# Kernel optimization log

Hardware: AMD Instinct MI355X
Metric: run time of the kernel (lower is better)

The kernel has to match this reference:

```python
import jax, jax.numpy as jnp
import numpy as np

B, L, D = 4, 896, 2048
HQ, HKV, HD = 32, 8, 64
GROUP = HQ // HKV          # 4
TOKENS_PER_FRAME = 7
ROPE_BASE = 10000.0


def setup_inputs() -> dict:
    key = jax.random.key(0)
    ks = jax.random.split(key, 5)
    s = 0.02
    return {
        "x": jax.random.normal(ks[0], (B, L, D), jnp.float32),
        "wq": jax.random.normal(ks[1], (D, D), jnp.float32) * s,
        "wk": jax.random.normal(ks[2], (D, HKV * HD), jnp.float32) * s,
        "wv": jax.random.normal(ks[3], (D, HKV * HD), jnp.float32) * s,
        "wo": jax.random.normal(ks[4], (D, D), jnp.float32) * s,
        "pos_ids": jnp.arange(L, dtype=jnp.int32),
    }


def _apply_rotary(t, cos, sin):
    # t: [B, L, H, HD]; rotate all HD dims, interleaved pairs.
    Bt, Lt, Ht, Hd = t.shape
    tp = t.reshape(Bt, Lt, Ht, Hd // 2, 2)
    x1, x2 = tp[..., 0], tp[..., 1]
    c = cos[None, :, None, :]   # [1, L, 1, HD/2]
    s = sin[None, :, None, :]
    y1 = x1 * c - x2 * s
    y2 = x1 * s + x2 * c
    return jnp.stack([y1, y2], axis=-1).reshape(Bt, Lt, Ht, Hd)


def reference(x, wq, wk, wv, wo, pos_ids):
    Bx, Lx, Dx = x.shape
    q = (x @ wq).reshape(Bx, Lx, HQ, HD)
    k = (x @ wk).reshape(Bx, Lx, HKV, HD)
    v = (x @ wv).reshape(Bx, Lx, HKV, HD)

    # RoPE (rot_dim = head_dim), scale = 1.0
    half = HD // 2
    inv_freq = 1.0 / (ROPE_BASE ** (jnp.arange(half, dtype=jnp.float32) / half))
    freqs = pos_ids.astype(jnp.float32)[:, None] * inv_freq[None, :]  # [L, HD/2]
    cos, sin = jnp.cos(freqs), jnp.sin(freqs)
    q = _apply_rotary(q, cos, sin)
    k = _apply_rotary(k, cos, sin)

    # GQA: expand kv heads to q heads (kv_head = q_head // GROUP)
    k = jnp.repeat(k, GROUP, axis=2)   # [B, L, HQ, HD]
    v = jnp.repeat(v, GROUP, axis=2)

    scale = 1.0 / jnp.sqrt(jnp.float32(HD))
    scores = jnp.einsum('blhd,bmhd->bhlm', q, k) * scale  # [B, HQ, L, L]

    # frame-block causal mask: allow key frame <= query frame
    pos = jnp.arange(Lx)
    fid = pos // TOKENS_PER_FRAME
    allow = fid[None, :] <= fid[:, None]                  # [L, L]
    neg = jnp.finfo(scores.dtype).min
    scores = jnp.where(allow[None, None], scores, neg)

    probs = jax.nn.softmax(scores, axis=-1)
    out = jnp.einsum('bhlm,bmhd->blhd', probs, v).reshape(Bx, Lx, Dx)
    return out @ wo
```

## Files before the change

### kernel.cpp

```cpp
#include <hip/hip_runtime.h>
#include <hip/hip_bf16.h>
#include <cstdint>

typedef __bf16 bf16;
typedef __bf16 bf16x8 __attribute__((ext_vector_type(8)));
typedef float floatx4 __attribute__((ext_vector_type(4)));

#define B_   4
#define L_   896
#define D_   2048
#define HQ_  32
#define HKV_ 8
#define HD_  64
#define NQKV 3072
#define M_   3584

__device__ inline void gl_lds16(const bf16* g, bf16* l) {
    __builtin_amdgcn_global_load_lds(
        (const __attribute__((address_space(1))) void*)g,
        (__attribute__((address_space(3))) void*)l, 16, 0, 0);
}

__device__ inline void barrier_() {
    asm volatile("" ::: "memory");
    __builtin_amdgcn_s_barrier();
    asm volatile("" ::: "memory");
}

__global__ __launch_bounds__(256) void convert_to_bf16(const float* __restrict__ in,
                                                       bf16* __restrict__ out) {
    long q = (long)blockIdx.x * 256 + threadIdx.x;
    float4 v = ((const float4*)in)[q];
    union { bf16 b[4]; ushort4 u; } w;
    w.b[0] = (bf16)v.x; w.b[1] = (bf16)v.y; w.b[2] = (bf16)v.z; w.b[3] = (bf16)v.w;
    ((ushort4*)out)[q] = w.u;
}

__global__ __launch_bounds__(256) void rope_cs_kernel(const int* __restrict__ pos_ids,
                                                      float2* __restrict__ cs) {
    int idx = blockIdx.x * 256 + threadIdx.x;
    if (idx >= L_ * 32) return;
    int l = idx >> 5, i = idx & 31;
    float p = (float)pos_ids[l];
    float inv = exp2f(-(float)i * (13.287712379549449f / 32.0f));
    float a = p * inv;
    cs[idx] = make_float2(cosf(a), sinf(a));
}

__global__ __launch_bounds__(256) void rope_apply(bf16* __restrict__ QKV,
                                                  const float2* __restrict__ cs) {
    int idx = blockIdx.x * 256 + threadIdx.x;
    int m = idx / 320, g = idx - m * 320;
    int l = m % L_;
    int hp = (g * 4) & 31;
    const float2* ct = &cs[l * 32 + hp];
    bf16* p = QKV + (long)m * NQKV + g * 8;
    bf16x8 v = *(bf16x8*)p;
    bf16x8 w;
#pragma unroll
    for (int i = 0; i < 4; i++) {
        float2 csv = ct[i];
        float x1 = (float)v[2 * i], x2 = (float)v[2 * i + 1];
        w[2 * i]     = (bf16)(x1 * csv.x - x2 * csv.y);
        w[2 * i + 1] = (bf16)(x1 * csv.y + x2 * csv.x);
    }
    *(bf16x8*)p = w;
}

__global__ __launch_bounds__(256) void transpose_cvt(
    const float* __restrict__ in, ushort* __restrict__ out, int C, int R) {
    __shared__ ushort t[64][72];
    int tid = threadIdx.x;
    int tr = tid >> 4, tc = (tid & 15) << 2;
    long r0 = (long)blockIdx.y << 6, c0 = (long)blockIdx.x << 6;
#pragma unroll
    for (int i = 0; i < 4; ++i) {
        float4 v = *(const float4*)&in[(r0 + tr + i * 16) * C + c0 + tc];
        union { bf16 b[4]; ushort4 u; } w;
        w.b[0] = (bf16)v.x; w.b[1] = (bf16)v.y; w.b[2] = (bf16)v.z; w.b[3] = (bf16)v.w;
        *(ushort4*)&t[tr + i * 16][tc] = w.u;
    }
    __syncthreads();
#pragma unroll
    for (int i = 0; i < 4; ++i) {
        ushort4 w;
        w.x = t[tc + 0][tr + i * 16];
        w.y = t[tc + 1][tr + i * 16];
        w.z = t[tc + 2][tr + i * 16];
        w.w = t[tc + 3][tr + i * 16];
        *(ushort4*)&out[(c0 + tr + i * 16) * R + r0 + tc] = w;
    }
}

__global__ __launch_bounds__(256) void transpose_u16(
    const ushort* __restrict__ in, ushort* __restrict__ out,
    int ld_in, int ld_out, long is1, long is2, long os1, long os2) {
    __shared__ ushort t[64][72];
    int z = blockIdx.z;
    const ushort* ip = in + (long)(z >> 3) * is1 + (long)(z & 7) * is2;
    ushort* op = out + (long)(z >> 3) * os1 + (long)(z & 7) * os2;
    int tid = threadIdx.x;
    int tr = tid >> 4, tc = (tid & 15) << 2;
    long r0 = (long)blockIdx.y << 6, c0 = (long)blockIdx.x << 6;
#pragma unroll
    for (int i = 0; i < 4; ++i) {
        ushort4 v = *(const ushort4*)&ip[(r0 + tr + i * 16) * ld_in + c0 + tc];
        *(ushort4*)&t[tr + i * 16][tc] = v;
    }
    __syncthreads();
#pragma unroll
    for (int i = 0; i < 4; ++i) {
        ushort4 w;
        w.x = t[tc + 0][tr + i * 16];
        w.y = t[tc + 1][tr + i * 16];
        w.z = t[tc + 2][tr + i * 16];
        w.w = t[tc + 3][tr + i * 16];
        *(ushort4*)&op[(c0 + tr + i * 16) * ld_out + r0 + tc] = w;
    }
}

template <int JF, int OUTF32>
__global__ __launch_bounds__(512, 2) void gemm224(
    const bf16* __restrict__ A, const bf16* __restrict__ Bt, void* __restrict__ C,
    int Ntot, int Ktot) {
    __shared__ bf16 ldsA[2][224 * 64];
    __shared__ bf16 ldsB[2][JF * 64 * 64];
    const int tid = threadIdx.x;
    const int lane = tid & 63;
    const int quad = lane >> 4, l16 = lane & 15;
    const int w = tid >> 6;
    const int wr = w >> 2, wc = w & 3;

    const int gx = gridDim.x;
    const int nwg = gx * gridDim.y;
    int orig = blockIdx.y * gx + blockIdx.x;
    int q8 = nwg >> 3, r8 = nwg & 7;
    int xcd = orig & 7, lid = orig >> 3;
    int wg = (xcd < r8 ? xcd * (q8 + 1) : r8 * (q8 + 1) + (xcd - r8) * q8) + lid;
    const long m0 = (long)(wg / gx) * 224;
    const long n0 = (long)(wg % gx) * (JF * 64);

    const long rowK = Ktot;
    const int srow = tid >> 3;
    const int scol = ((tid & 7) ^ (srow & 7)) << 3;
    const bf16* baseA = A  + (m0 + srow) * rowK + scol;
    const bf16* baseB = Bt + (n0 + srow) * rowK + scol;
    bf16* const dA = (bf16*)ldsA + tid * 8;
    bf16* const dB = (bf16*)ldsB + tid * 8;

    const int m7 = l16 & 7;
    const int col0 = ((0 + quad) ^ m7) << 3;
    const int col1 = ((4 + quad) ^ m7) << 3;
    const int abase = wr * 112 + l16;
    const int bbase = wc * (JF * 16) + l16;

    floatx4 acc[7][JF];
#pragma unroll
    for (int i = 0; i < 7; ++i)
#pragma unroll
        for (int j = 0; j < JF; ++j)
#pragma unroll
            for (int r = 0; r < 4; ++r) acc[i][j][r] = 0.f;

    bf16x8 af0[4][2], af1[3][2], bq[JF][2];

    const int T = Ktot >> 6;

    {
        gl_lds16(baseA,              dA);
        gl_lds16(baseA + 64 * rowK,  dA + 4096);
        gl_lds16(baseA + 128 * rowK, dA + 8192);
        if (tid < 256) gl_lds16(baseA + 192 * rowK, dA + 12288);
#pragma unroll
        for (int r = 0; r < JF; ++r) gl_lds16(baseB + r * 64 * rowK, dB + r * 4096);
#pragma unroll
        for (int r = 0; r < JF; ++r) gl_lds16(baseB + 64 + r * 64 * rowK,
                                              dB + JF * 4096 + r * 4096);
    }
    if (JF == 3) asm volatile("s_waitcnt vmcnt(3)" ::: "memory");
    else         asm volatile("s_waitcnt vmcnt(2)" ::: "memory");
    barrier_();

    for (int t = 0; t < T; ++t) {
        const int cur = t & 1, nxt = cur ^ 1;
        const bf16* pa = &ldsA[cur][0];
        const bf16* pb = &ldsB[cur][0];
        const long koff  = (long)(t + 1) * 64;
        const long koff2 = (long)(t + 2) * 64;

#pragma unroll
        for (int i = 0; i < 4; ++i) {
            const bf16* rp = &pa[(abase + i * 16) * 64];
            af0[i][0] = *(const bf16x8*)&rp[col0];
            af0[i][1] = *(const bf16x8*)&rp[col1];
        }
#pragma unroll
        for (int j = 0; j < JF; ++j) {
            const bf16* rp = &pb[(bbase + j * 16) * 64];
            bq[j][0] = *(const bf16x8*)&rp[col0];
            bq[j][1] = *(const bf16x8*)&rp[col1];
        }
        if (t + 1 < T) {
            const bf16* g = baseA + koff;
            bf16* l = dA + nxt * (224 * 64);
            gl_lds16(g,              l);
            gl_lds16(g + 64 * rowK,  l + 4096);
            gl_lds16(g + 128 * rowK, l + 8192);
            if (tid < 256) gl_lds16(g + 192 * rowK, l + 12288);
        }
        barrier_();
        asm volatile("s_waitcnt lgkmcnt(0)" ::: "memory");
        __builtin_amdgcn_sched_barrier(0);
        __builtin_amdgcn_s_setprio(1);
#pragma unroll
        for (int i = 0; i < 4; ++i)
#pragma unroll
            for (int j = 0; j < JF; ++j) {
                floatx4 c = acc[i][j];
                c = __builtin_amdgcn_mfma_f32_16x16x32_bf16(af0[i][0], bq[j][0], c, 0, 0, 0);
                c = __builtin_amdgcn_mfma_f32_16x16x32_bf16(af0[i][1], bq[j][1], c, 0, 0, 0);
                acc[i][j] = c;
            }
        __builtin_amdgcn_s_setprio(0);
        barrier_();

#pragma unroll
        for (int i = 0; i < 3; ++i) {
            const bf16* rp = &pa[(abase + (4 + i) * 16) * 64];
            af1[i][0] = *(const bf16x8*)&rp[col0];
            af1[i][1] = *(const bf16x8*)&rp[col1];
        }
        if (t + 2 < T) {
            const bf16* g = baseB + koff2;
            bf16* l = dB + cur * (JF * 64 * 64);
#pragma unroll
            for (int r = 0; r < JF; ++r) gl_lds16(g + r * 64 * rowK, l + r * 4096);
        }
        barrier_();
        asm volatile("s_waitcnt lgkmcnt(0)" ::: "memory");
        __builtin_amdgcn_sched_barrier(0);
        __builtin_amdgcn_s_setprio(1);
#pragma unroll
        for (int i = 0; i < 3; ++i)
#pragma unroll
            for (int j = 0; j < JF; ++j) {
                floatx4 c = acc[4 + i][j];
                c = __builtin_amdgcn_mfma_f32_16x16x32_bf16(af1[i][0], bq[j][0], c, 0, 0, 0);
                c = __builtin_amdgcn_mfma_f32_16x16x32_bf16(af1[i][1], bq[j][1], c, 0, 0, 0);
                acc[4 + i][j] = c;
            }
        __builtin_amdgcn_s_setprio(0);
        if (t + 2 < T) {
            if (JF == 3) asm volatile("s_waitcnt vmcnt(3)" ::: "memory");
            else         asm volatile("s_waitcnt vmcnt(2)" ::: "memory");
        } else {
            asm volatile("s_waitcnt vmcnt(0)" ::: "memory");
        }
        barrier_();
    }

#pragma unroll
    for (int i = 0; i < 7; ++i)
#pragma unroll
        for (int j = 0; j < JF; ++j)
#pragma unroll
            for (int r = 0; r < 4; ++r) {
                long m = m0 + wr * 112 + i * 16 + quad * 4 + r;
                long n = n0 + wc * (JF * 16) + j * 16 + l16;
                if (OUTF32) ((float*)C)[m * Ntot + n] = acc[i][j][r];
                else        ((bf16*)C)[m * Ntot + n] = (bf16)acc[i][j][r];
            }
}

__global__ __launch_bounds__(512) void attn_kernel(
    const bf16* __restrict__ QKV,
    const bf16* __restrict__ Vt,
    bf16* __restrict__ AO) {
    __shared__ bf16 Ks[64 * 72];
    __shared__ bf16 Vs[64 * 72];
    __shared__ bf16 Ps[8][32 * 72];
    const int tid  = threadIdx.x;
    const int wid  = tid >> 6, lane = tid & 63;
    const int quad = lane >> 4, c = lane & 15;
    const int b = blockIdx.z, kvh = blockIdx.y;
    const int hq = kvh * 4 + (wid >> 1);
    const int sub = wid & 1;
    const int xpair = blockIdx.x;
    bf16* ps = &Ps[wid][0];

    const bf16* Kb = QKV + ((long)(b * L_)) * NQKV + D_ + kvh * HD_;
    const bf16* Vb = Vt + ((long)(b * HKV_ + kvh)) * (HD_ * L_);

    const int srow = tid >> 3, schunk = (tid & 7) << 3;
    const bf16* kp = &Kb[(long)srow * NQKV + schunk];
    const bf16* vp = &Vb[(long)srow * L_ + schunk];

    const floatx4 fzero = {0.f, 0.f, 0.f, 0.f};
    const float C1 = 0.18033688011112042f;

#pragma unroll 1
    for (int pass = 0; pass < 2; ++pass) {
        const int x = pass == 0 ? xpair : 13 - xpair;
        const int q0b = x * 64;
        const bf16* Qb = QKV + ((long)(b * L_ + q0b + sub * 32)) * NQKV + hq * HD_;

        bf16x8 qf[2][2];
#pragma unroll
        for (int a = 0; a < 2; a++) {
            qf[a][0] = *(const bf16x8*)&Qb[(long)(a * 16 + c) * NQKV + quad * 8];
            qf[a][1] = *(const bf16x8*)&Qb[(long)(a * 16 + c) * NQKV + 32 + quad * 8];
        }

        float lsum[2][4];
        floatx4 o[2][4];
#pragma unroll
        for (int a = 0; a < 2; a++)
#pragma unroll
            for (int r = 0; r < 4; r++) lsum[a][r] = 0.f;
#pragma unroll
        for (int a = 0; a < 2; a++)
#pragma unroll
            for (int nt = 0; nt < 4; nt++)
#pragma unroll
                for (int r = 0; r < 4; r++) o[a][nt][r] = 0.f;

        int fe[2][4];
#pragma unroll
        for (int a = 0; a < 2; a++)
#pragma unroll
            for (int r = 0; r < 4; r++) {
                int l = q0b + sub * 32 + a * 16 + quad * 4 + r;
                fe[a][r] = (l / 7 + 1) * 7;
            }
        const int femin = (q0b / 7 + 1) * 7;
        const int kend  = ((q0b + 63) / 7 + 1) * 7;

        bf16x8 kg = *(const bf16x8*)&kp[0];
        bf16x8 vg = *(const bf16x8*)&vp[0];

        for (int k0 = 0; k0 < kend; k0 += 64) {
            __syncthreads();
            *(bf16x8*)&Ks[srow * 72 + schunk] = kg;
            *(bf16x8*)&Vs[srow * 72 + schunk] = vg;
            __syncthreads();

            const int kn = k0 + 64;
            if (kn < kend) {
                kg = *(const bf16x8*)&kp[(long)kn * NQKV];
                vg = *(const bf16x8*)&vp[kn];
            }

            bf16x8 kf[4][2];
#pragma unroll
            for (int n = 0; n < 4; n++) {
                kf[n][0] = *(bf16x8*)&Ks[(n * 16 + c) * 72 + quad * 8];
                kf[n][1] = *(bf16x8*)&Ks[(n * 16 + c) * 72 + 32 + quad * 8];
            }
            const int masked = (k0 + 64 > femin);
#pragma unroll
            for (int a = 0; a < 2; a++) {
                floatx4 s[4];
#pragma unroll
                for (int n = 0; n < 4; n++) {
                    s[n] = __builtin_amdgcn_mfma_f32_16x16x32_bf16(qf[a][0], kf[n][0], fzero, 0, 0, 0);
                    s[n] = __builtin_amdgcn_mfma_f32_16x16x32_bf16(qf[a][1], kf[n][1], s[n], 0, 0, 0);
                }
                if (masked) {
#pragma unroll
                    for (int n = 0; n < 4; n++) {
                        const int key = k0 + n * 16 + c;
#pragma unroll
                        for (int r = 0; r < 4; r++) {
                            float e = exp2f(s[n][r] * C1);
                            e = (key < fe[a][r]) ? e : 0.f;
                            lsum[a][r] += e;
                            ps[(a * 16 + quad * 4 + r) * 72 + n * 16 + c] = (bf16)e;
                        }
                    }
                } else {
#pragma unroll
                    for (int n = 0; n < 4; n++) {
#pragma unroll
                        for (int r = 0; r < 4; r++) {
                            float e = exp2f(s[n][r] * C1);
                            lsum[a][r] += e;
                            ps[(a * 16 + quad * 4 + r) * 72 + n * 16 + c] = (bf16)e;
                        }
                    }
                }
            }
            bf16x8 vf[4][2];
#pragma unroll
            for (int nt = 0; nt < 4; nt++) {
                vf[nt][0] = *(bf16x8*)&Vs[(nt * 16 + c) * 72 + quad * 8];
                vf[nt][1] = *(bf16x8*)&Vs[(nt * 16 + c) * 72 + 32 + quad * 8];
            }
#pragma unroll
            for (int a = 0; a < 2; a++) {
                bf16x8 pf0 = *(bf16x8*)&ps[(a * 16 + c) * 72 + quad * 8];
                bf16x8 pf1 = *(bf16x8*)&ps[(a * 16 + c) * 72 + 32 + quad * 8];
#pragma unroll
                for (int nt = 0; nt < 4; nt++) {
                    o[a][nt] = __builtin_amdgcn_mfma_f32_16x16x32_bf16(pf0, vf[nt][0], o[a][nt], 0, 0, 0);
                    o[a][nt] = __builtin_amdgcn_mfma_f32_16x16x32_bf16(pf1, vf[nt][1], o[a][nt], 0, 0, 0);
                }
            }
        }
#pragma unroll
        for (int a = 0; a < 2; a++)
#pragma unroll
            for (int r = 0; r < 4; r++) {
#pragma unroll
                for (int off = 1; off < 16; off <<= 1)
                    lsum[a][r] += __shfl_xor(lsum[a][r], off);
            }
#pragma unroll
        for (int a = 0; a < 2; a++)
#pragma unroll
            for (int nt = 0; nt < 4; nt++)
#pragma unroll
                for (int r = 0; r < 4; r++) {
                    int l = q0b + sub * 32 + a * 16 + quad * 4 + r;
                    AO[((long)(b * L_ + l)) * D_ + hq * HD_ + nt * 16 + c] =
                        (bf16)(o[a][nt][r] / lsum[a][r]);
                }
    }
}

extern "C" void kernel_launch(void* const* d_in, const int* in_sizes, int n_in,
                              void* d_out, int out_size, void* d_ws, size_t ws_size,
                              hipStream_t stream) {
    (void)in_sizes; (void)n_in; (void)out_size; (void)ws_size;
    const float* x  = (const float*)d_in[0];
    const float* wq = (const float*)d_in[1];
    const float* wk = (const float*)d_in[2];
    const float* wv = (const float*)d_in[3];
    const float* wo = (const float*)d_in[4];
    const int* pos  = (const int*)d_in[5];

    bf16* ws    = (bf16*)d_ws;
    bf16* xb    = ws;
    bf16* wqkvT = ws + 7340032L;
    bf16* woT   = ws + 13631488L;
    bf16* QKV   = ws + 17825792L;
    bf16* Vt    = ws + 28835840L;
    bf16* AO    = xb;
    float2* cs  = (float2*)(ws + 30670848L);

    convert_to_bf16<<<dim3(7168), 256, 0, stream>>>(x, xb);
    rope_cs_kernel<<<dim3(112), dim3(256), 0, stream>>>(pos, cs);

    transpose_cvt<<<dim3(32, 32), 256, 0, stream>>>(wq, (ushort*)wqkvT, 2048, 2048);
    transpose_cvt<<<dim3(8, 32), 256, 0, stream>>>(wk, (ushort*)(wqkvT + 4194304L), 512, 2048);
    transpose_cvt<<<dim3(8, 32), 256, 0, stream>>>(wv, (ushort*)(wqkvT + 5242880L), 512, 2048);
    transpose_cvt<<<dim3(32, 32), 256, 0, stream>>>(wo, (ushort*)woT, 2048, 2048);

    gemm224<3, 0><<<dim3(16, 16), 512, 0, stream>>>(xb, wqkvT, QKV, NQKV, D_);

    rope_apply<<<dim3(4480), 256, 0, stream>>>(QKV, cs);

    transpose_u16<<<dim3(1, 14, 32), 256, 0, stream>>>(
        (const ushort*)(QKV + 2560), (ushort*)Vt, 3072, 896,
        896L * 3072, 64, 8L * 57344, 57344);

    attn_kernel<<<dim3(7, 8, 4), 512, 0, stream>>>(QKV, Vt, AO);

    gemm224<2, 1><<<dim3(16, 16), 512, 0, stream>>>(AO, woT, d_out, D_, D_);
}
```

Measured before the change: 258.9 us.

## Split attention blocks into two head-pairs and swizzle K/V shared memory

The attention kernel now launches 256-thread blocks covering two query heads each, doubling the grid so more blocks spread across compute units. Each thread loads two rows of K and V per tile. Padded K/V shared arrays are replaced with an XOR-swizzled 64-wide layout, and the P buffer pitch changes to 76, to cut LDS bank conflicts. The cost is that each K/V tile is now loaded twice from global memory, once per head-pair block.

Result: slower. 269.6 us (+4.1%).

```diff
diff --git a/kernel.cpp b/kernel.cpp
--- a/kernel.cpp
+++ b/kernel.cpp
@@ -272,18 +272,19 @@
             }
 }
 
-__global__ __launch_bounds__(512) void attn_kernel(
+__global__ __launch_bounds__(256) void attn_kernel(
     const bf16* __restrict__ QKV,
     const bf16* __restrict__ Vt,
     bf16* __restrict__ AO) {
-    __shared__ bf16 Ks[64 * 72];
-    __shared__ bf16 Vs[64 * 72];
-    __shared__ bf16 Ps[8][32 * 72];
+    __shared__ bf16 Ks[64 * 64];
+    __shared__ bf16 Vs[64 * 64];
+    __shared__ bf16 Ps[4][32 * 76];
     const int tid  = threadIdx.x;
     const int wid  = tid >> 6, lane = tid & 63;
     const int quad = lane >> 4, c = lane & 15;
-    const int b = blockIdx.z, kvh = blockIdx.y;
-    const int hq = kvh * 4 + (wid >> 1);
+    const int b = blockIdx.z;
+    const int kvh = blockIdx.y >> 1, hp = blockIdx.y & 1;
+    const int hq = kvh * 4 + hp * 2 + (wid >> 1);
     const int sub = wid & 1;
     const int xpair = blockIdx.x;
     bf16* ps = &Ps[wid][0];
@@ -292,8 +293,15 @@
     const bf16* Vb = Vt + ((long)(b * HKV_ + kvh)) * (HD_ * L_);
 
     const int srow = tid >> 3, schunk = (tid & 7) << 3;
-    const bf16* kp = &Kb[(long)srow * NQKV + schunk];
-    const bf16* vp = &Vb[(long)srow * L_ + schunk];
+    const int sslot = ((tid & 7) ^ (srow & 7)) << 3;
+    const bf16* kp0 = &Kb[(long)srow * NQKV + schunk];
+    const bf16* kp1 = &Kb[(long)(32 + srow) * NQKV + schunk];
+    const bf16* vp0 = &Vb[(long)srow * L_ + schunk];
+    const bf16* vp1 = &Vb[(long)(srow + 32) * L_ + schunk];
+
+    const int m7 = c & 7;
+    const int col0 = ((0 + quad) ^ m7) << 3;
+    const int col1 = ((4 + quad) ^ m7) << 3;
 
     const floatx4 fzero = {0.f, 0.f, 0.f, 0.f};
     const float C1 = 0.18033688011112042f;
@@ -335,26 +343,33 @@
         const int femin = (q0b / 7 + 1) * 7;
         const int kend  = ((q0b + 63) / 7 + 1) * 7;
 
-        bf16x8 kg = *(const bf16x8*)&kp[0];
-        bf16x8 vg = *(const bf16x8*)&vp[0];
+        bf16x8 kg0 = *(const bf16x8*)&kp0[0];
+        bf16x8 kg1 = *(const bf16x8*)&kp1[0];
+        bf16x8 vg0 = *(const bf16x8*)&vp0[0];
+        bf16x8 vg1 = *(const bf16x8*)&vp1[0];
 
         for (int k0 = 0; k0 < kend; k0 += 64) {
             __syncthreads();
-            *(bf16x8*)&Ks[srow * 72 + schunk] = kg;
-            *(bf16x8*)&Vs[srow * 72 + schunk] = vg;
+            *(bf16x8*)&Ks[srow * 64 + sslot]        = kg0;
+            *(bf16x8*)&Ks[(srow + 32) * 64 + sslot] = kg1;
+            *(bf16x8*)&Vs[srow * 64 + sslot]        = vg0;
+            *(bf16x8*)&Vs[(srow + 32) * 64 + sslot] = vg1;
             __syncthreads();
 
             const int kn = k0 + 64;
             if (kn < kend) {
-                kg = *(const bf16x8*)&kp[(long)kn * NQKV];
-                vg = *(const bf16x8*)&vp[kn];
+                kg0 = *(const bf16x8*)&kp0[(long)kn * NQKV];
+                kg1 = *(const bf16x8*)&kp1[(long)kn * NQKV];
+                vg0 = *(const bf16x8*)&vp0[kn];
+                vg1 = *(const bf16x8*)&vp1[kn];
             }
 
             bf16x8 kf[4][2];
 #pragma unroll
             for (int n = 0; n < 4; n++) {
-                kf[n][0] = *(bf16x8*)&Ks[(n * 16 + c) * 72 + quad * 8];
-                kf[n][1] = *(bf16x8*)&Ks[(n * 16 + c) * 72 + 32 + quad * 8];
+                const bf16* rp = &Ks[(n * 16 + c) * 64];
+                kf[n][0] = *(bf16x8*)&rp[col0];
+                kf[n][1] = *(bf16x8*)&rp[col1];
             }
             const int masked = (k0 + 64 > femin);
 #pragma unroll
@@ -374,7 +389,7 @@
                             float e = exp2f(s[n][r] * C1);
                             e = (key < fe[a][r]) ? e : 0.f;
                             lsum[a][r] += e;
-                            ps[(a * 16 + quad * 4 + r) * 72 + n * 16 + c] = (bf16)e;
+                            ps[(a * 16 + quad * 4 + r) * 76 + n * 16 + c] = (bf16)e;
                         }
                     }
                 } else {
@@ -384,7 +399,7 @@
                         for (int r = 0; r < 4; r++) {
                             float e = exp2f(s[n][r] * C1);
                             lsum[a][r] += e;
-                            ps[(a * 16 + quad * 4 + r) * 72 + n * 16 + c] = (bf16)e;
+                            ps[(a * 16 + quad * 4 + r) * 76 + n * 16 + c] = (bf16)e;
                         }
                     }
                 }
@@ -392,13 +407,14 @@
             bf16x8 vf[4][2];
 #pragma unroll
             for (int nt = 0; nt < 4; nt++) {
-                vf[nt][0] = *(bf16x8*)&Vs[(nt * 16 + c) * 72 + quad * 8];
-                vf[nt][1] = *(bf16x8*)&Vs[(nt * 16 + c) * 72 + 32 + quad * 8];
+                const bf16* rp = &Vs[(nt * 16 + c) * 64];
+                vf[nt][0] = *(bf16x8*)&rp[col0];
+                vf[nt][1] = *(bf16x8*)&rp[col1];
             }
 #pragma unroll
             for (int a = 0; a < 2; a++) {
-                bf16x8 pf0 = *(bf16x8*)&ps[(a * 16 + c) * 72 + quad * 8];
-                bf16x8 pf1 = *(bf16x8*)&ps[(a * 16 + c) * 72 + 32 + quad * 8];
+                bf16x8 pf0 = *(bf16x8*)&ps[(a * 16 + c) * 76 + quad * 8];
+                bf16x8 pf1 = *(bf16x8*)&ps[(a * 16 + c) * 76 + 32 + quad * 8];
 #pragma unroll
                 for (int nt = 0; nt < 4; nt++) {
                     o[a][nt] = __builtin_amdgcn_mfma_f32_16x16x32_bf16(pf0, vf[nt][0], o[a][nt], 0, 0, 0);
@@ -463,7 +479,7 @@
         (const ushort*)(QKV + 2560), (ushort*)Vt, 3072, 896,
         896L * 3072, 64, 8L * 57344, 57344);
 
-    attn_kernel<<<dim3(7, 8, 4), 512, 0, stream>>>(QKV, Vt, AO);
+    attn_kernel<<<dim3(7, 16, 4), 256, 0, stream>>>(QKV, Vt, AO);
 
     gemm224<2, 1><<<dim3(16, 16), 512, 0, stream>>>(AO, woT, d_out, D_, D_);
 }
```
